# Kernel tuning notes

Hardware: AMD Instinct MI355X
Metric: run time of the kernel (lower is better)

The kernel has to match this reference:

```python
import jax, jax.numpy as jnp
import numpy as np

DIM = 512
HEADS = 8
DIM_HEAD = 64
INNER = HEADS * DIM_HEAD          # 512
CPB_DIM = DIM // 2                # 256 (ContinuousPositionBias hidden dim)
FF_INNER = int(DIM * 4 * 2 / 3)   # 1365 (GEGLU inner dim)
B, C, F, H, W = 2, 512, 8, 32, 32
SCALE = DIM_HEAD ** -0.5


def setup_inputs() -> dict:
    key = jax.random.key(0)
    ks = jax.random.split(key, 24)
    def rnd(k, shape, s=0.02):
        return jax.random.normal(k, shape, jnp.float32) * s
    return {
        "x": jax.random.normal(ks[0], (B, C, F, W, W), jnp.float32)[:, :, :, :H, :],
        # spatial attention
        "sa_gamma": jnp.ones((DIM,), jnp.float32),
        "sa_wq": rnd(ks[1], (DIM, INNER)),
        "sa_wkv": rnd(ks[2], (DIM, 2 * INNER)),
        "sa_wo": rnd(ks[3], (INNER, DIM)),
        # temporal attention
        "ta_gamma": jnp.ones((DIM,), jnp.float32),
        "ta_wq": rnd(ks[4], (DIM, INNER)),
        "ta_wkv": rnd(ks[5], (DIM, 2 * INNER)),
        "ta_wo": rnd(ks[6], (INNER, DIM)),
        # spatial ContinuousPositionBias MLP (num_dims=2, layers=2)
        "sp_w1": rnd(ks[7], (2, CPB_DIM), 0.1), "sp_b1": jnp.zeros((CPB_DIM,), jnp.float32),
        "sp_w2": rnd(ks[8], (CPB_DIM, CPB_DIM), 0.05), "sp_b2": jnp.zeros((CPB_DIM,), jnp.float32),
        "sp_w3": rnd(ks[9], (CPB_DIM, HEADS), 0.05), "sp_b3": jnp.zeros((HEADS,), jnp.float32),
        # temporal ContinuousPositionBias MLP (num_dims=1)
        "tp_w1": rnd(ks[10], (1, CPB_DIM), 0.1), "tp_b1": jnp.zeros((CPB_DIM,), jnp.float32),
        "tp_w2": rnd(ks[11], (CPB_DIM, CPB_DIM), 0.05), "tp_b2": jnp.zeros((CPB_DIM,), jnp.float32),
        "tp_w3": rnd(ks[12], (CPB_DIM, HEADS), 0.05), "tp_b3": jnp.zeros((HEADS,), jnp.float32),
        # FeedForward: Conv3d 1x1 (no bias) -> GEGLU -> RMSNorm -> Conv3d 1x1
        "ff_win": rnd(ks[13], (DIM, 2 * FF_INNER)),
        "ff_gamma": jnp.ones((FF_INNER,), jnp.float32),
        "ff_wout": rnd(ks[14], (FF_INNER, DIM)),
    }


def _rms_last(x, g):
    # torch: F.normalize(x, dim=-1) * sqrt(C) * gamma
    nrm = jnp.sqrt(jnp.sum(x * x, axis=-1, keepdims=True))
    return x / jnp.maximum(nrm, 1e-12) * jnp.sqrt(jnp.float32(x.shape[-1])) * g


def _mlp_bias(rel, w1, b1, w2, b2, w3, b3):
    h = jax.nn.silu(rel @ w1 + b1)
    h = jax.nn.silu(h @ w2 + b2)
    return h @ w3 + b3  # [R, heads]


def _cpb_2d(h, w, params):
    ry = jnp.arange(-(h - 1), h, dtype=jnp.float32)
    rx = jnp.arange(-(w - 1), w, dtype=jnp.float32)
    gy, gx = jnp.meshgrid(ry, rx, indexing='ij')
    rel = jnp.stack([gy, gx], -1).reshape(-1, 2)          # [(2h-1)(2w-1), 2]
    tab = _mlp_bias(rel, *params)                          # [R, heads]
    py, px = jnp.meshgrid(jnp.arange(h), jnp.arange(w), indexing='ij')
    pos = jnp.stack([py.reshape(-1), px.reshape(-1)], -1)  # [n, 2]
    d = pos[:, None, :] - pos[None, :, :]                  # [n, n, 2]
    idx = (d[..., 0] + h - 1) * (2 * w - 1) + (d[..., 1] + w - 1)
    return jnp.transpose(tab[idx], (2, 0, 1))              # [heads, n, n]


def _cpb_1d(f, params):
    rel = jnp.arange(-(f - 1), f, dtype=jnp.float32)[:, None]
    tab = _mlp_bias(rel, *params)                          # [2f-1, heads]
    p = jnp.arange(f)
    idx = p[:, None] - p[None, :] + f - 1
    return jnp.transpose(tab[idx], (2, 0, 1))              # [heads, f, f]


def _attn(x, gamma, wq, wkv, wo, bias):
    # x: [b, n, c]; manual softmax(QK^T*scale + bias)V (flash disabled by pos_bias)
    xn = _rms_last(x, gamma)
    q = xn @ wq
    k, v = jnp.split(xn @ wkv, 2, axis=-1)
    b, n, _ = q.shape
    rs = lambda t: t.reshape(b, n, HEADS, DIM_HEAD).transpose(0, 2, 1, 3)
    q, k, v = rs(q), rs(k), rs(v)
    s = jnp.einsum('bhid,bhjd->bhij', q, k) * SCALE + bias[None]
    a = jax.nn.softmax(s, axis=-1)
    o = jnp.einsum('bhij,bhjd->bhid', a, v)
    o = o.transpose(0, 2, 1, 3).reshape(b, n, INNER)
    return o @ wo


def _ff(x, win, gamma, wout):
    # x: [b, f, h, w, c] channel-last; Conv3d 1x1 == channel einsum
    hdn = jnp.einsum('bfhwc,co->bfhwo', x, win)
    a, gate = jnp.split(hdn, 2, axis=-1)
    y = a * jax.nn.gelu(gate, approximate=False)           # GEGLU (torch exact gelu)
    # shift_token: chunk channels, shift second half by +1 frame
    c1 = (FF_INNER + 1) // 2
    t1, t2 = y[..., :c1], y[..., c1:]
    t2 = jnp.pad(t2, ((0, 0), (1, 0), (0, 0), (0, 0), (0, 0)))[:, :-1]
    y = jnp.concatenate([t1, t2], axis=-1)
    yn = _rms_last(y, gamma)                               # RMSNorm over channels
    return jnp.einsum('bfhwi,ic->bfhwc', yn, wout)


def reference(x, sa_gamma, sa_wq, sa_wkv, sa_wo, ta_gamma, ta_wq, ta_wkv, ta_wo,
              sp_w1, sp_b1, sp_w2, sp_b2, sp_w3, sp_b3,
              tp_w1, tp_b1, tp_w2, tp_b2, tp_w3, tp_b3,
              ff_win, ff_gamma, ff_wout):
    b, c, f, h, w = x.shape
    xl = jnp.transpose(x, (0, 2, 3, 4, 1))                 # b f h w c
    # spatial attention over (h w) tokens, batched over (b f)
    xs = xl.reshape(b * f, h * w, c)
    sp_bias = _cpb_2d(h, w, (sp_w1, sp_b1, sp_w2, sp_b2, sp_w3, sp_b3))
    xs = _attn(xs, sa_gamma, sa_wq, sa_wkv, sa_wo, sp_bias) + xs
    xv = xs.reshape(b, f, h, w, c)
    # temporal attention over f tokens, batched over (b h w)
    xt = jnp.transpose(xv, (0, 2, 3, 1, 4)).reshape(b * h * w, f, c)
    tp_bias = _cpb_1d(f, (tp_w1, tp_b1, tp_w2, tp_b2, tp_w3, tp_b3))
    xt = _attn(xt, ta_gamma, ta_wq, ta_wkv, ta_wo, tp_bias) + xt
    xv = jnp.transpose(xt.reshape(b, h, w, f, c), (0, 3, 1, 2, 4))
    # GEGLU feedforward with token shift
    xv = _ff(xv, ff_win, ff_gamma, ff_wout) + xv
    return jnp.transpose(xv, (0, 4, 1, 2, 3))              # b c f h w
```

## Files before the change

kernel.cpp:

```cpp
#include <hip/hip_runtime.h>
#include <cstdint>
#include <cstddef>

typedef __bf16 bf16_t;
typedef __bf16 bf16x8 __attribute__((ext_vector_type(8)));
typedef __bf16 bf16x4 __attribute__((ext_vector_type(4)));
typedef float floatx4 __attribute__((ext_vector_type(4)));

__device__ __forceinline__ float wred_sum(float v) {
#pragma unroll
  for (int off = 32; off > 0; off >>= 1) v += __shfl_xor(v, off);
  return v;
}
__device__ __forceinline__ void async16(const void* g, void* l) {
  __builtin_amdgcn_global_load_lds((const __attribute__((address_space(1))) void*)g,
                                   (__attribute__((address_space(3))) void*)l, 16, 0, 0);
}

template <int MODE>
__global__ __launch_bounds__(256) void st_gemm(
    const bf16_t* __restrict__ A, const bf16_t* __restrict__ B, void* Cp, void* Cp2,
    const float* Res, int M, int N, int K, int lda, int ldb, int ldc) {
  __shared__ bf16_t sA[3][128 * 32];
  __shared__ bf16_t sB[3][128 * 32];
  const int tid = threadIdx.x;
  const int bm = blockIdx.x, bn = blockIdx.y;
  const int lane = tid & 63;
  const int wave = tid >> 6;
  const int wm = (wave >> 1) * 64, wn = (wave & 1) * 64;
  const int rowf = lane & 15, qc = lane >> 4;
  const int fco = (qc ^ ((rowf >> 1) & 3)) * 8;

  const bf16_t* aSrc[2];
  const bf16_t* bSrc[2];
  int sOff[2];
#pragma unroll
  for (int it = 0; it < 2; ++it) {
    int slot = it * 256 + tid;
    int mi = slot >> 2, kc = slot & 3;
    int cs = kc ^ ((mi >> 1) & 3);
    int ar = bm * 128 + mi; if (ar > M - 1) ar = M - 1;
    int br = bn * 128 + mi; if (br > N - 1) br = N - 1;
    aSrc[it] = A + (size_t)ar * lda + cs * 8;
    bSrc[it] = B + (size_t)br * ldb + cs * 8;
    sOff[it] = slot * 16;
  }

  floatx4 acc[4][4];
#pragma unroll
  for (int i = 0; i < 4; ++i)
#pragma unroll
    for (int j = 0; j < 4; ++j) acc[i][j] = floatx4{0.f, 0.f, 0.f, 0.f};

  const int NT = K >> 5;
#pragma unroll
  for (int it = 0; it < 2; ++it) {
    async16(aSrc[it], (char*)sA[0] + sOff[it]);
    async16(bSrc[it], (char*)sB[0] + sOff[it]);
  }
#pragma unroll
  for (int it = 0; it < 2; ++it) {
    async16(aSrc[it] + 32, (char*)sA[1] + sOff[it]);
    async16(bSrc[it] + 32, (char*)sB[1] + sOff[it]);
  }
  __builtin_amdgcn_sched_barrier(0);
  asm volatile("s_waitcnt vmcnt(4)" ::: "memory");
  __builtin_amdgcn_s_barrier();
  __builtin_amdgcn_sched_barrier(0);

  int bcur = 0, bnx = 2;
#pragma unroll 1
  for (int t = 0; t < NT; ++t) {
    const bf16_t* sAc = sA[bcur];
    const bf16_t* sBc = sB[bcur];
    bf16x8 af[4], bv[4];
#pragma unroll
    for (int i = 0; i < 4; ++i) {
      af[i] = *(const bf16x8*)(sAc + (wm + i * 16 + rowf) * 32 + fco);
      bv[i] = *(const bf16x8*)(sBc + (wn + i * 16 + rowf) * 32 + fco);
    }
    if (t + 2 < NT) {
      const int kt2 = (t + 2) * 32;
#pragma unroll
      for (int it = 0; it < 2; ++it) {
        async16(aSrc[it] + kt2, (char*)sA[bnx] + sOff[it]);
        async16(bSrc[it] + kt2, (char*)sB[bnx] + sOff[it]);
      }
    }
#pragma unroll
    for (int i = 0; i < 4; ++i)
#pragma unroll
      for (int j = 0; j < 4; ++j)
        acc[i][j] = __builtin_amdgcn_mfma_f32_16x16x32_bf16(af[i], bv[j], acc[i][j], 0, 0, 0);
    if (t + 1 < NT) {
      __builtin_amdgcn_sched_barrier(0);
      if (t + 2 < NT) asm volatile("s_waitcnt vmcnt(4)" ::: "memory");
      else            asm volatile("s_waitcnt vmcnt(0)" ::: "memory");
      __builtin_amdgcn_s_barrier();
      __builtin_amdgcn_sched_barrier(0);
    }
    bcur = (bcur == 2) ? 0 : bcur + 1;
    bnx = (bnx == 2) ? 0 : bnx + 1;
  }

  const int cl = lane & 15;
  const int rowBase = bm * 128 + wm + (lane >> 4) * 4;
  if (MODE == 5) {
    bf16_t* yb = (bf16_t*)Cp;
    const int cg0 = ((bn * 128 + wn) >> 5) * 16;
#pragma unroll
    for (int i = 0; i < 4; ++i) {
#pragma unroll
      for (int p = 0; p < 2; ++p) {
        int c = cg0 + p * 16 + cl;
        if (c >= 1365) continue;
#pragma unroll
        for (int r = 0; r < 4; ++r) {
          int row = rowBase + i * 16 + r;
          if (row >= M) continue;
          float a = acc[i][2 * p][r];
          float gt = acc[i][2 * p + 1][r];
          float zz = gt * (0.7978845608f + 0.03567740814f * gt * gt);
          float u = __builtin_exp2f(-2.8853900817779268f * zz);
          float y = a * gt / (1.f + u);
          yb[(size_t)row * ldc + c] = (bf16_t)y;
        }
      }
    }
    return;
  }
  const int colBase = bn * 128 + wn + cl;
#pragma unroll
  for (int i = 0; i < 4; ++i) {
#pragma unroll
    for (int j = 0; j < 4; ++j) {
      int col = colBase + j * 16;
      if (col >= N) continue;
#pragma unroll
      for (int r = 0; r < 4; ++r) {
        int row = rowBase + i * 16 + r;
        if (row >= M) continue;
        long long inidx = (long long)row * ldc + col;
        float v = acc[i][j][r];
        if (MODE >= 2) v += Res[inidx];
        if (MODE == 1) { ((bf16_t*)Cp)[inidx] = (bf16_t)v; }
        else if (MODE == 2) { ((float*)Cp)[inidx] = v; }
        else if (MODE == 3) {
          int orow = (row & ~8191) | ((row & 1023) << 3) | ((row >> 10) & 7);
          ((float*)Cp)[(long long)orow * ldc + col] = v;
        } else if (MODE == 4) {
          int orow = (row & ~8191) | ((row & 7) << 10) | ((row >> 3) & 1023);
          long long oidx = (long long)orow * ldc + col;
          ((float*)Cp)[oidx] = v;
          ((bf16_t*)Cp2)[oidx] = (bf16_t)v;
        }
      }
    }
  }
}

__global__ __launch_bounds__(256) void st_transpose2d(
    const float* __restrict__ in, float* __restrict__ out, int R, int Cc,
    long long inb, long long outb) {
  __shared__ float tile[32][33];
  const int ct = blockIdx.x, rt = blockIdx.y, b = blockIdx.z;
  in += (long long)b * inb;
  out += (long long)b * outb;
  const int tx = threadIdx.x & 31, ty = threadIdx.x >> 5;
#pragma unroll
  for (int k = 0; k < 4; ++k) {
    int r = rt * 32 + ty + k * 8;
    int c = ct * 32 + tx;
    tile[ty + k * 8][tx] = in[(size_t)r * Cc + c];
  }
  __syncthreads();
#pragma unroll
  for (int k = 0; k < 4; ++k) {
    int c = ct * 32 + ty + k * 8;
    int r = rt * 32 + tx;
    out[(size_t)c * R + r] = tile[tx][ty + k * 8];
  }
}

__global__ void st_wtrans(const float* __restrict__ src, bf16_t* __restrict__ dst,
                          int K, int Kpad, int N, int srcld, int coloff, long total) {
  long idx = (long)blockIdx.x * 256 + threadIdx.x;
  if (idx >= total) return;
  int kp = (int)(idx % Kpad);
  int n = (int)(idx / Kpad);
  float v = (kp < K) ? src[(size_t)kp * srcld + coloff + n] : 0.f;
  dst[idx] = (bf16_t)v;
}

__global__ void st_wtrans_geglu(const float* __restrict__ src, bf16_t* __restrict__ dst,
                                long total) {
  long idx = (long)blockIdx.x * 256 + threadIdx.x;
  if (idx >= total) return;
  int kp = (int)(idx & 511);
  int n = (int)(idx >> 9);
  int c = ((n >> 5) << 4) + (n & 15);
  float v = 0.f;
  if (c < 1365) {
    int srccol = c + (((n >> 4) & 1) ? 1365 : 0);
    v = src[(size_t)kp * 2730 + srccol];
  }
  dst[idx] = (bf16_t)v;
}

__global__ __launch_bounds__(256) void st_cpb(
    const float* __restrict__ w1, const float* __restrict__ b1,
    const float* __restrict__ w2, const float* __restrict__ b2,
    const float* __restrict__ w3, const float* __restrict__ b3,
    float* __restrict__ tab2d, float* __restrict__ tab1d, int two_d) {
  const int pos = blockIdx.x, t = threadIdx.x;
  float r0, r1 = 0.f;
  if (two_d) { r0 = (float)(pos / 63 - 31); r1 = (float)(pos % 63 - 31); }
  else { r0 = (float)(pos - 7); }
  __shared__ float sh[256];
  float h = r0 * w1[t] + (two_d ? r1 * w1[256 + t] : 0.f) + b1[t];
  h = h / (1.f + expf(-h));
  sh[t] = h;
  __syncthreads();
  float h2 = b2[t];
  for (int j = 0; j < 256; ++j) h2 += sh[j] * w2[j * 256 + t];
  h2 = h2 / (1.f + expf(-h2));
  __syncthreads();
  sh[t] = h2;
  __syncthreads();
  if (t < 8) {
    float o = b3[t];
    for (int j = 0; j < 256; ++j) o += sh[j] * w3[j * 8 + t];
    if (two_d) tab2d[t * 4000 + pos] = o * 8.0f;
    else tab1d[t * 15 + pos] = o;
  }
}

__global__ __launch_bounds__(256) void st_rmsnorm(const float* __restrict__ x,
                                                  const float* __restrict__ gamma,
                                                  bf16_t* __restrict__ y) {
  const int token = blockIdx.x * 4 + (threadIdx.x >> 6);
  const int lane = threadIdx.x & 63;
  const float* xr = x + (size_t)token * 512;
  float v[8];
  float ss = 0.f;
#pragma unroll
  for (int k = 0; k < 8; ++k) { v[k] = xr[k * 64 + lane]; ss += v[k] * v[k]; }
  ss = wred_sum(ss);
  const float r = 22.627416998f / fmaxf(sqrtf(ss), 1e-12f);
  bf16_t* yr = y + (size_t)token * 512;
#pragma unroll
  for (int k = 0; k < 8; ++k) yr[k * 64 + lane] = (bf16_t)(v[k] * r * gamma[k * 64 + lane]);
}

__global__ __launch_bounds__(256) void st_vtrans(const bf16_t* __restrict__ qkv,
                                                 bf16_t* __restrict__ vT) {
  __shared__ float tile[32][33];
  const int jt = blockIdx.x, dt = blockIdx.y, z = blockIdx.z;
  const int bf = z >> 3, h = z & 7;
  const int tx = threadIdx.x & 31, ty = threadIdx.x >> 5;
#pragma unroll
  for (int k = 0; k < 4; ++k) {
    int j = jt * 32 + ty + k * 8;
    int d = dt * 32 + tx;
    tile[ty + k * 8][tx] = (float)qkv[((size_t)(bf * 1024 + j)) * 1536 + 1024 + h * 64 + d];
  }
  __syncthreads();
#pragma unroll
  for (int k = 0; k < 4; ++k) {
    int d = dt * 32 + ty + k * 8;
    int j = jt * 32 + tx;
    vT[((size_t)z * 64 + d) * 1024 + j] = (bf16_t)tile[tx][ty + k * 8];
  }
}

__global__ __launch_bounds__(256, 4) void st_flash(
    const bf16_t* __restrict__ qkv, const bf16_t* __restrict__ vT,
    const float* __restrict__ tab2f, bf16_t* __restrict__ ob) {
  __shared__ __align__(16) bf16_t ldsK[3][32 * 64];
  __shared__ __align__(16) char ldsP[4 * 32 * 80];
  __shared__ __align__(16) float ldsT[2208];
  const int z = blockIdx.x;
  const int qtile = blockIdx.y;
  const int bf = z >> 3, h = z & 7;
  const int tid = threadIdx.x;
  const int lane = tid & 63, wave = tid >> 6;
  const int cl = lane & 15, g = lane >> 4;
  const size_t qkvBase = (size_t)bf * 1024 * 1536 + h * 64;
  const int eoff = (qtile * 252) & ~3;
  const bf16_t* Kp = qkv + qkvBase + 512;
  const bf16_t* Vp = vT + (size_t)z * 65536;

#pragma unroll
  for (int it = 0; it < 3; ++it) {
    int s = it * 256 + tid;
    if (s < 552) async16(tab2f + h * 4000 + eoff + s * 4, (char*)ldsT + s * 16);
  }
  const int krow = tid >> 3, kc = tid & 7;
  const bf16_t* kSrc = Kp + (size_t)krow * 1536 + (kc ^ (krow & 7)) * 8;
  async16(kSrc, (char*)ldsK[0] + tid * 16);
  async16(kSrc + (size_t)32 * 1536, (char*)ldsK[1] + tid * 16);
  bf16x8 aq[2][2];
#pragma unroll
  for (int it = 0; it < 2; ++it)
#pragma unroll
    for (int ks = 0; ks < 2; ++ks) {
      int row = qtile * 128 + wave * 32 + it * 16 + cl;
      aq[it][ks] = *(const bf16x8*)(qkv + qkvBase + (size_t)row * 1536 + (ks * 4 + g) * 8);
    }
  const bf16_t* vPtr[4];
#pragma unroll
  for (int dt = 0; dt < 4; ++dt) vPtr[dt] = Vp + (size_t)(dt * 16 + cl) * 1024 + g * 8;
  __syncthreads();

  int fiB[2];
#pragma unroll
  for (int it = 0; it < 2; ++it) {
    int i = qtile * 128 + wave * 32 + it * 16 + cl;
    fiB[it] = (i >> 5) * 63 + (i & 31) + 1984 - eoff;
  }
  float lsum[2] = {0.f, 0.f};
  floatx4 oacc[4][2];
#pragma unroll
  for (int dt = 0; dt < 4; ++dt)
#pragma unroll
    for (int it = 0; it < 2; ++it) oacc[dt][it] = floatx4{0.f, 0.f, 0.f, 0.f};

  char* ldsPw = ldsP + wave * 2560;
  const float SC = 0.18033688011112042f;

  int bcur = 0, bnx = 2;
#pragma unroll 1
  for (int t = 0; t < 32; ++t) {
    const bf16_t* Kc = ldsK[bcur];
    const int j0 = t * 32;
#pragma unroll
    for (int jt = 0; jt < 2; ++jt) {
      int jb = j0 + jt * 16 + g * 4;
      int fjb = (jb >> 5) * 63 + (jb & 31);
      floatx4 sj[2];
#pragma unroll
      for (int it = 0; it < 2; ++it) {
        int idx0 = fiB[it] - fjb;
        sj[it] = floatx4{ldsT[idx0], ldsT[idx0 - 1], ldsT[idx0 - 2], ldsT[idx0 - 3]};
      }
#pragma unroll
      for (int ks = 0; ks < 2; ++ks) {
        int row = jt * 16 + cl;
        bf16x8 kf = *(const bf16x8*)(Kc + row * 64 + (((ks * 4 + g) ^ (row & 7))) * 8);
#pragma unroll
        for (int it = 0; it < 2; ++it)
          sj[it] = __builtin_amdgcn_mfma_f32_16x16x32_bf16(kf, aq[it][ks], sj[it], 0, 0, 0);
      }
#pragma unroll
      for (int it = 0; it < 2; ++it) {
        float e0 = __builtin_exp2f(sj[it][0] * SC);
        float e1 = __builtin_exp2f(sj[it][1] * SC);
        float e2 = __builtin_exp2f(sj[it][2] * SC);
        float e3 = __builtin_exp2f(sj[it][3] * SC);
        lsum[it] += (e0 + e1) + (e2 + e3);
        bf16x4 pv = {(bf16_t)e0, (bf16_t)e1, (bf16_t)e2, (bf16_t)e3};
        *(bf16x4*)(ldsPw + (it * 16 + cl) * 80 + (jt * 4 + g) * 8) = pv;
      }
    }
    {
      bf16x8 pB[2];
#pragma unroll
      for (int it = 0; it < 2; ++it)
        pB[it] = *(const bf16x8*)(ldsPw + (it * 16 + cl) * 80 + g * 16);
#pragma unroll
      for (int dt = 0; dt < 4; ++dt) {
        bf16x8 vf = *(const bf16x8*)(vPtr[dt] + j0);
#pragma unroll
        for (int it = 0; it < 2; ++it)
          oacc[dt][it] = __builtin_amdgcn_mfma_f32_16x16x32_bf16(vf, pB[it], oacc[dt][it], 0, 0, 0);
      }
    }
    if (t + 2 < 32) async16(kSrc + (size_t)(t + 2) * 32 * 1536, (char*)ldsK[bnx] + tid * 16);
    if (t + 1 < 32) {
      __builtin_amdgcn_sched_barrier(0);
      if (t + 2 < 32) asm volatile("s_waitcnt vmcnt(1)" ::: "memory");
      else            asm volatile("s_waitcnt vmcnt(0)" ::: "memory");
      __builtin_amdgcn_s_barrier();
      __builtin_amdgcn_sched_barrier(0);
    }
    bcur = (bcur == 2) ? 0 : bcur + 1;
    bnx = (bnx == 2) ? 0 : bnx + 1;
  }
  float inv[2];
#pragma unroll
  for (int it = 0; it < 2; ++it) {
    float s = lsum[it];
    s += __shfl_xor(s, 16);
    s += __shfl_xor(s, 32);
    inv[it] = 1.f / s;
  }
#pragma unroll
  for (int it = 0; it < 2; ++it) {
    int i = qtile * 128 + wave * 32 + it * 16 + cl;
    size_t base = ((size_t)bf * 1024 + i) * 512 + h * 64 + g * 4;
#pragma unroll
    for (int dt = 0; dt < 4; ++dt) {
      bf16x4 ov = {(bf16_t)(oacc[dt][it][0] * inv[it]), (bf16_t)(oacc[dt][it][1] * inv[it]),
                   (bf16_t)(oacc[dt][it][2] * inv[it]), (bf16_t)(oacc[dt][it][3] * inv[it])};
      *(bf16x4*)(ob + base + dt * 16) = ov;
    }
  }
}

__global__ __launch_bounds__(256) void st_tattn2(const bf16_t* __restrict__ qkv,
                                                 const float* __restrict__ tabf,
                                                 bf16_t* __restrict__ o) {
  const int wg = blockIdx.x * 4 + (threadIdx.x >> 6);
  const int bhw = wg >> 3, head = wg & 7;
  const int lane = threadIdx.x & 63;
  const size_t base = (size_t)bhw * 8 * 1536 + head * 64 + lane;
  float q[8], k[8], v[8];
#pragma unroll
  for (int f = 0; f < 8; ++f) {
    q[f] = (float)qkv[base + (size_t)f * 1536];
    k[f] = (float)qkv[base + (size_t)f * 1536 + 512];
    v[f] = (float)qkv[base + (size_t)f * 1536 + 1024];
  }
  float p[64];
#pragma unroll
  for (int i = 0; i < 8; ++i)
#pragma unroll
    for (int j = 0; j < 8; ++j) p[i * 8 + j] = q[i] * k[j];
#pragma unroll
  for (int st = 32; st >= 1; st >>= 1) {
    const bool hi = (lane & st) != 0;
#pragma unroll
    for (int m = 0; m < st; ++m) {
      float give = hi ? p[m] : p[m + st];
      float keep = hi ? p[m + st] : p[m];
      p[m] = keep + __shfl_xor(give, st);
    }
  }
  const int i = lane >> 3, j = lane & 7;
  float e = __expf(p[0] * 0.125f + tabf[head * 15 + i - j + 7]);
  float sm = e;
  sm += __shfl_xor(sm, 1);
  sm += __shfl_xor(sm, 2);
  sm += __shfl_xor(sm, 4);
  const float prob = e / sm;
  float acc[8];
#pragma unroll
  for (int ii = 0; ii < 8; ++ii) acc[ii] = 0.f;
#pragma unroll
  for (int ii = 0; ii < 8; ++ii)
#pragma unroll
    for (int jj = 0; jj < 8; ++jj)
      acc[ii] += __shfl(prob, ii * 8 + jj) * v[jj];
#pragma unroll
  for (int ii = 0; ii < 8; ++ii)
    o[(size_t)(bhw * 8 + ii) * 512 + head * 64 + lane] = (bf16_t)acc[ii];
}

__global__ __launch_bounds__(256) void st_glu(const bf16_t* __restrict__ y,
                                              const float* __restrict__ gamma,
                                              bf16_t* __restrict__ yn) {
  const int t = blockIdx.x;
  const int tid = threadIdx.x;
  const int f = (t >> 10) & 7;
  float yv[6];
  float ss = 0.f;
#pragma unroll
  for (int kk = 0; kk < 6; ++kk) {
    int c = kk * 256 + tid;
    float v = 0.f;
    if (c < 1365) {
      long src = t;
      bool valid = true;
      if (c >= 683) { if (f == 0) valid = false; else src = t - 1024; }
      if (valid) v = (float)y[src * 1365 + c];
    }
    yv[kk] = v;
    ss += v * v;
  }
  __shared__ float red[4];
  ss = wred_sum(ss);
  if ((tid & 63) == 0) red[tid >> 6] = ss;
  __syncthreads();
  ss = red[0] + red[1] + red[2] + red[3];
  const float r = sqrtf(1365.f) / fmaxf(sqrtf(ss), 1e-12f);
#pragma unroll
  for (int kk = 0; kk < 6; ++kk) {
    int c = kk * 256 + tid;
    if (c < 1365) yn[(size_t)t * 1376 + c] = (bf16_t)(yv[kk] * r * gamma[c]);
  }
  if (tid < 11) yn[(size_t)t * 1376 + 1365 + tid] = (bf16_t)0.f;
}

extern "C" void kernel_launch(void* const* d_in, const int* in_sizes, int n_in,
                              void* d_out, int out_size, void* d_ws, size_t ws_size,
                              hipStream_t stream) {
  const float* x        = (const float*)d_in[0];
  const float* sa_gamma = (const float*)d_in[1];
  const float* sa_wq    = (const float*)d_in[2];
  const float* sa_wkv   = (const float*)d_in[3];
  const float* sa_wo    = (const float*)d_in[4];
  const float* ta_gamma = (const float*)d_in[5];
  const float* ta_wq    = (const float*)d_in[6];
  const float* ta_wkv   = (const float*)d_in[7];
  const float* ta_wo    = (const float*)d_in[8];
  const float* sp_w1 = (const float*)d_in[9];
  const float* sp_b1 = (const float*)d_in[10];
  const float* sp_w2 = (const float*)d_in[11];
  const float* sp_b2 = (const float*)d_in[12];
  const float* sp_w3 = (const float*)d_in[13];
  const float* sp_b3 = (const float*)d_in[14];
  const float* tp_w1 = (const float*)d_in[15];
  const float* tp_b1 = (const float*)d_in[16];
  const float* tp_w2 = (const float*)d_in[17];
  const float* tp_b2 = (const float*)d_in[18];
  const float* tp_w3 = (const float*)d_in[19];
  const float* tp_b3 = (const float*)d_in[20];
  const float* ff_win   = (const float*)d_in[21];
  const float* ff_gamma = (const float*)d_in[22];
  const float* ff_wout  = (const float*)d_in[23];
  float* outp = (float*)d_out;

  char* ws = (char*)d_ws;
  size_t off = 0;
  auto alloc = [&](size_t bytes) -> char* {
    char* p = ws + off;
    off += (bytes + 255) & ~(size_t)255;
    return p;
  };
  const long T = 16384;
  float*  xs  = (float*)alloc((size_t)T * 512 * 4);
  bf16_t* xn  = (bf16_t*)alloc((size_t)T * 512 * 2);
  char*   R2  = alloc((size_t)T * 1536 * 2);
  char*   R3  = alloc((size_t)T * 1536 * 2);
  char*   R4  = alloc((size_t)T * 1376 * 2);
  bf16_t* wqkvT_sa = (bf16_t*)alloc(1536ULL * 512 * 2);
  bf16_t* woT_sa   = (bf16_t*)alloc(512ULL * 512 * 2);
  bf16_t* wqkvT_ta = (bf16_t*)alloc(1536ULL * 512 * 2);
  bf16_t* woT_ta   = (bf16_t*)alloc(512ULL * 512 * 2);
  bf16_t* winT  = (bf16_t*)alloc(2752ULL * 512 * 2);
  bf16_t* woutT = (bf16_t*)alloc(512ULL * 1376 * 2);
  float*  tab2f = (float*)alloc(8 * 4000 * 4);
  float*  tabf  = (float*)alloc(8 * 15 * 4);

  bf16_t* qkv  = (bf16_t*)R2;
  bf16_t* ybuf = (bf16_t*)R2;
  bf16_t* vT   = (bf16_t*)R3;
  float*  xt   = (float*)R3;
  bf16_t* ob_s = xn;
  bf16_t* ob_t = (bf16_t*)R4;
  bf16_t* ynb  = (bf16_t*)R4;

  st_transpose2d<<<dim3(256, 16, 2), 256, 0, stream>>>(x, xs, 512, 8192,
                                                       (long long)512 * 8192, (long long)512 * 8192);
  auto wt = [&](const float* src, bf16_t* dst, int K, int Kpad, int N, int srcld, int coloff) {
    long tot = (long)N * Kpad;
    st_wtrans<<<dim3((tot + 255) / 256), 256, 0, stream>>>(src, dst, K, Kpad, N, srcld, coloff, tot);
  };
  wt(sa_wq, wqkvT_sa, 512, 512, 512, 512, 0);
  wt(sa_wkv, wqkvT_sa + 512 * 512, 512, 512, 1024, 1024, 0);
  wt(sa_wo, woT_sa, 512, 512, 512, 512, 0);
  wt(ta_wq, wqkvT_ta, 512, 512, 512, 512, 0);
  wt(ta_wkv, wqkvT_ta + 512 * 512, 512, 512, 1024, 1024, 0);
  wt(ta_wo, woT_ta, 512, 512, 512, 512, 0);
  st_wtrans_geglu<<<dim3((2752 * 512) / 256), 256, 0, stream>>>(ff_win, winT, 2752L * 512);
  wt(ff_wout, woutT, 1365, 1376, 512, 512, 0);
  st_cpb<<<dim3(3969), 256, 0, stream>>>(sp_w1, sp_b1, sp_w2, sp_b2, sp_w3, sp_b3, tab2f, tabf, 1);
  st_cpb<<<dim3(15), 256, 0, stream>>>(tp_w1, tp_b1, tp_w2, tp_b2, tp_w3, tp_b3, tab2f, tabf, 0);

  st_rmsnorm<<<dim3(4096), 256, 0, stream>>>(xs, sa_gamma, xn);
  st_gemm<1><<<dim3(128, 12), 256, 0, stream>>>(
      xn, wqkvT_sa, (void*)qkv, nullptr, nullptr, 16384, 1536, 512, 512, 512, 1536);
  st_vtrans<<<dim3(32, 2, 128), 256, 0, stream>>>(qkv, vT);
  st_flash<<<dim3(128, 8), 256, 0, stream>>>(qkv, vT, tab2f, ob_s);
  st_gemm<3><<<dim3(128, 4), 256, 0, stream>>>(
      ob_s, woT_sa, (void*)xt, nullptr, xs, 16384, 512, 512, 512, 512, 512);

  st_rmsnorm<<<dim3(4096), 256, 0, stream>>>(xt, ta_gamma, xn);
  st_gemm<1><<<dim3(128, 12), 256, 0, stream>>>(
      xn, wqkvT_ta, (void*)qkv, nullptr, nullptr, 16384, 1536, 512, 512, 512, 1536);
  st_tattn2<<<dim3(4096), 256, 0, stream>>>(qkv, tabf, ob_t);
  st_gemm<4><<<dim3(128, 4), 256, 0, stream>>>(
      ob_t, woT_ta, (void*)xs, (void*)xn, xt, 16384, 512, 512, 512, 512, 512);

  st_gemm<5><<<dim3(128, 22), 256, 0, stream>>>(
      xn, winT, (void*)ybuf, nullptr, nullptr, 16384, 2752, 512, 512, 512, 1365);
  st_glu<<<dim3(16384), 256, 0, stream>>>(ybuf, ff_gamma, ynb);
  st_gemm<2><<<dim3(128, 4), 256, 0, stream>>>(
      ynb, woutT, (void*)xs, nullptr, xs, 16384, 512, 1376, 1376, 1376, 512);

  st_transpose2d<<<dim3(16, 256, 2), 256, 0, stream>>>(xs, outp, 8192, 512,
                                                       (long long)8192 * 512, (long long)8192 * 512);
}
```

Baseline: 658.0 us.

## Use wider 128x256 GEMM tile for GEGLU projection and fold softmax scale into Q

Adds a dedicated GEGLU input-projection GEMM with a 128x256 output tile (4x8 MFMA accumulators per wave, launch bounds of 2 blocks per CU). It takes over from the 128x128 MODE 5 path, with the weight padding enlarged to 2816 rows. This aims to improve operand reuse per LDS load and cut the block count. Separately, the attention scale times log2(e) is now applied to Q in the QKV GEMM epilogue, and the position-bias tables are pre-multiplied by log2(e), which removes per-score multiplies in both attention kernels. The wider tile raises register pressure and can limit occupancy, and scaling Q before the bf16 rounding slightly changes numerics.

```diff
diff --git a/kernel.cpp b/kernel.cpp
--- a/kernel.cpp
+++ b/kernel.cpp
@@ -16,6 +16,8 @@
   __builtin_amdgcn_global_load_lds((const __attribute__((address_space(1))) void*)g,
                                    (__attribute__((address_space(3))) void*)l, 16, 0, 0);
 }
+
+#define QSCALE 0.18033688011112042f
 
 template <int MODE>
 __global__ __launch_bounds__(256) void st_gemm(
@@ -105,30 +107,6 @@
 
   const int cl = lane & 15;
   const int rowBase = bm * 128 + wm + (lane >> 4) * 4;
-  if (MODE == 5) {
-    bf16_t* yb = (bf16_t*)Cp;
-    const int cg0 = ((bn * 128 + wn) >> 5) * 16;
-#pragma unroll
-    for (int i = 0; i < 4; ++i) {
-#pragma unroll
-      for (int p = 0; p < 2; ++p) {
-        int c = cg0 + p * 16 + cl;
-        if (c >= 1365) continue;
-#pragma unroll
-        for (int r = 0; r < 4; ++r) {
-          int row = rowBase + i * 16 + r;
-          if (row >= M) continue;
-          float a = acc[i][2 * p][r];
-          float gt = acc[i][2 * p + 1][r];
-          float zz = gt * (0.7978845608f + 0.03567740814f * gt * gt);
-          float u = __builtin_exp2f(-2.8853900817779268f * zz);
-          float y = a * gt / (1.f + u);
-          yb[(size_t)row * ldc + c] = (bf16_t)y;
-        }
-      }
-    }
-    return;
-  }
   const int colBase = bn * 128 + wn + cl;
 #pragma unroll
   for (int i = 0; i < 4; ++i) {
@@ -142,8 +120,9 @@
         if (row >= M) continue;
         long long inidx = (long long)row * ldc + col;
         float v = acc[i][j][r];
-        if (MODE >= 2) v += Res[inidx];
+        if (MODE >= 2 && MODE <= 4) v += Res[inidx];
         if (MODE == 1) { ((bf16_t*)Cp)[inidx] = (bf16_t)v; }
+        else if (MODE == 6) { ((bf16_t*)Cp)[inidx] = (bf16_t)(col < 512 ? v * QSCALE : v); }
         else if (MODE == 2) { ((float*)Cp)[inidx] = v; }
         else if (MODE == 3) {
           int orow = (row & ~8191) | ((row & 1023) << 3) | ((row >> 10) & 7);
@@ -154,6 +133,119 @@
           ((float*)Cp)[oidx] = v;
           ((bf16_t*)Cp2)[oidx] = (bf16_t)v;
         }
+      }
+    }
+  }
+}
+
+__global__ __launch_bounds__(256, 2) void st_gemmW(
+    const bf16_t* __restrict__ A, const bf16_t* __restrict__ B, bf16_t* __restrict__ yb,
+    int M, int N, int K, int lda, int ldb, int ldc) {
+  __shared__ bf16_t sA[3][128 * 32];
+  __shared__ bf16_t sB[3][256 * 32];
+  const int tid = threadIdx.x;
+  const int bm = blockIdx.x, bn = blockIdx.y;
+  const int lane = tid & 63;
+  const int wave = tid >> 6;
+  const int wr = wave >> 1, wc = wave & 1;
+  const int rowf = lane & 15, qc = lane >> 4;
+  const int fco = (qc ^ ((rowf >> 1) & 3)) * 8;
+
+  const bf16_t* aSrc[2];
+  const bf16_t* bSrc[4];
+  int aOff[2], bOff[4];
+#pragma unroll
+  for (int it = 0; it < 2; ++it) {
+    int slot = it * 256 + tid;
+    int mi = slot >> 2, kc = slot & 3;
+    int cs = kc ^ ((mi >> 1) & 3);
+    aSrc[it] = A + (size_t)(bm * 128 + mi) * lda + cs * 8;
+    aOff[it] = slot * 16;
+  }
+#pragma unroll
+  for (int it = 0; it < 4; ++it) {
+    int slot = it * 256 + tid;
+    int mi = slot >> 2, kc = slot & 3;
+    int cs = kc ^ ((mi >> 1) & 3);
+    int br = bn * 256 + mi; if (br > N - 1) br = N - 1;
+    bSrc[it] = B + (size_t)br * ldb + cs * 8;
+    bOff[it] = slot * 16;
+  }
+
+  floatx4 acc[4][8];
+#pragma unroll
+  for (int i = 0; i < 4; ++i)
+#pragma unroll
+    for (int j = 0; j < 8; ++j) acc[i][j] = floatx4{0.f, 0.f, 0.f, 0.f};
+
+  const int NT = K >> 5;
+#pragma unroll
+  for (int tt = 0; tt < 2; ++tt) {
+#pragma unroll
+    for (int it = 0; it < 2; ++it) async16(aSrc[it] + tt * 32, (char*)sA[tt] + aOff[it]);
+#pragma unroll
+    for (int it = 0; it < 4; ++it) async16(bSrc[it] + tt * 32, (char*)sB[tt] + bOff[it]);
+  }
+  __builtin_amdgcn_sched_barrier(0);
+  asm volatile("s_waitcnt vmcnt(6)" ::: "memory");
+  __builtin_amdgcn_s_barrier();
+  __builtin_amdgcn_sched_barrier(0);
+
+  int bcur = 0, bnx = 2;
+#pragma unroll 1
+  for (int t = 0; t < NT; ++t) {
+    const bf16_t* sAc = sA[bcur];
+    const bf16_t* sBc = sB[bcur];
+    bf16x8 af[4], bv[8];
+#pragma unroll
+    for (int i = 0; i < 4; ++i)
+      af[i] = *(const bf16x8*)(sAc + (wr * 64 + i * 16 + rowf) * 32 + fco);
+#pragma unroll
+    for (int j = 0; j < 8; ++j)
+      bv[j] = *(const bf16x8*)(sBc + (wc * 128 + j * 16 + rowf) * 32 + fco);
+    if (t + 2 < NT) {
+      const int kt2 = (t + 2) * 32;
+#pragma unroll
+      for (int it = 0; it < 2; ++it) async16(aSrc[it] + kt2, (char*)sA[bnx] + aOff[it]);
+#pragma unroll
+      for (int it = 0; it < 4; ++it) async16(bSrc[it] + kt2, (char*)sB[bnx] + bOff[it]);
+    }
+    __builtin_amdgcn_s_setprio(1);
+#pragma unroll
+    for (int i = 0; i < 4; ++i)
+#pragma unroll
+      for (int j = 0; j < 8; ++j)
+        acc[i][j] = __builtin_amdgcn_mfma_f32_16x16x32_bf16(af[i], bv[j], acc[i][j], 0, 0, 0);
+    __builtin_amdgcn_s_setprio(0);
+    if (t + 1 < NT) {
+      __builtin_amdgcn_sched_barrier(0);
+      if (t + 2 < NT) asm volatile("s_waitcnt vmcnt(6)" ::: "memory");
+      else            asm volatile("s_waitcnt vmcnt(0)" ::: "memory");
+      __builtin_amdgcn_s_barrier();
+      __builtin_amdgcn_sched_barrier(0);
+    }
+    bcur = (bcur == 2) ? 0 : bcur + 1;
+    bnx = (bnx == 2) ? 0 : bnx + 1;
+  }
+
+  const int cl = lane & 15, g = lane >> 4;
+  const int rowBase = bm * 128 + wr * 64 + g * 4;
+  const int cg0 = (bn * 8 + wc * 4) * 16;
+#pragma unroll
+  for (int i = 0; i < 4; ++i) {
+#pragma unroll
+    for (int p = 0; p < 4; ++p) {
+      int c = cg0 + p * 16 + cl;
+      if (c >= 1365) continue;
+#pragma unroll
+      for (int r = 0; r < 4; ++r) {
+        int row = rowBase + i * 16 + r;
+        float a = acc[i][2 * p][r];
+        float gt = acc[i][2 * p + 1][r];
+        float zz = gt * (0.7978845608f + 0.03567740814f * gt * gt);
+        float u = __builtin_exp2f(-2.8853900817779268f * zz);
+        float y = a * gt / (1.f + u);
+        yb[(size_t)row * ldc + c] = (bf16_t)y;
       }
     }
   }
@@ -230,8 +322,8 @@
   if (t < 8) {
     float o = b3[t];
     for (int j = 0; j < 256; ++j) o += sh[j] * w3[j * 8 + t];
-    if (two_d) tab2d[t * 4000 + pos] = o * 8.0f;
-    else tab1d[t * 15 + pos] = o;
+    if (two_d) tab2d[t * 4000 + pos] = o * 1.4426950408889634f;
+    else tab1d[t * 15 + pos] = o * 1.4426950408889634f;
   }
 }
 
@@ -326,7 +418,6 @@
     for (int it = 0; it < 2; ++it) oacc[dt][it] = floatx4{0.f, 0.f, 0.f, 0.f};
 
   char* ldsPw = ldsP + wave * 2560;
-  const float SC = 0.18033688011112042f;
 
   int bcur = 0, bnx = 2;
 #pragma unroll 1
@@ -353,10 +444,10 @@
       }
 #pragma unroll
       for (int it = 0; it < 2; ++it) {
-        float e0 = __builtin_exp2f(sj[it][0] * SC);
-        float e1 = __builtin_exp2f(sj[it][1] * SC);
-        float e2 = __builtin_exp2f(sj[it][2] * SC);
-        float e3 = __builtin_exp2f(sj[it][3] * SC);
+        float e0 = __builtin_exp2f(sj[it][0]);
+        float e1 = __builtin_exp2f(sj[it][1]);
+        float e2 = __builtin_exp2f(sj[it][2]);
+        float e3 = __builtin_exp2f(sj[it][3]);
         lsum[it] += (e0 + e1) + (e2 + e3);
         bf16x4 pv = {(bf16_t)e0, (bf16_t)e1, (bf16_t)e2, (bf16_t)e3};
         *(bf16x4*)(ldsPw + (it * 16 + cl) * 80 + (jt * 4 + g) * 8) = pv;
@@ -437,7 +528,7 @@
     }
   }
   const int i = lane >> 3, j = lane & 7;
-  float e = __expf(p[0] * 0.125f + tabf[head * 15 + i - j + 7]);
+  float e = __builtin_exp2f(p[0] + tabf[head * 15 + i - j + 7]);
   float sm = e;
   sm += __shfl_xor(sm, 1);
   sm += __shfl_xor(sm, 2);
@@ -537,7 +628,7 @@
   bf16_t* woT_sa   = (bf16_t*)alloc(512ULL * 512 * 2);
   bf16_t* wqkvT_ta = (bf16_t*)alloc(1536ULL * 512 * 2);
   bf16_t* woT_ta   = (bf16_t*)alloc(512ULL * 512 * 2);
-  bf16_t* winT  = (bf16_t*)alloc(2752ULL * 512 * 2);
+  bf16_t* winT  = (bf16_t*)alloc(2816ULL * 512 * 2);
   bf16_t* woutT = (bf16_t*)alloc(512ULL * 1376 * 2);
   float*  tab2f = (float*)alloc(8 * 4000 * 4);
   float*  tabf  = (float*)alloc(8 * 15 * 4);
@@ -562,13 +653,13 @@
   wt(ta_wq, wqkvT_ta, 512, 512, 512, 512, 0);
   wt(ta_wkv, wqkvT_ta + 512 * 512, 512, 512, 1024, 1024, 0);
   wt(ta_wo, woT_ta, 512, 512, 512, 512, 0);
-  st_wtrans_geglu<<<dim3((2752 * 512) / 256), 256, 0, stream>>>(ff_win, winT, 2752L * 512);
+  st_wtrans_geglu<<<dim3((2816 * 512) / 256), 256, 0, stream>>>(ff_win, winT, 2816L * 512);
   wt(ff_wout, woutT, 1365, 1376, 512, 512, 0);
   st_cpb<<<dim3(3969), 256, 0, stream>>>(sp_w1, sp_b1, sp_w2, sp_b2, sp_w3, sp_b3, tab2f, tabf, 1);
   st_cpb<<<dim3(15), 256, 0, stream>>>(tp_w1, tp_b1, tp_w2, tp_b2, tp_w3, tp_b3, tab2f, tabf, 0);
 
   st_rmsnorm<<<dim3(4096), 256, 0, stream>>>(xs, sa_gamma, xn);
-  st_gemm<1><<<dim3(128, 12), 256, 0, stream>>>(
+  st_gemm<6><<<dim3(128, 12), 256, 0, stream>>>(
       xn, wqkvT_sa, (void*)qkv, nullptr, nullptr, 16384, 1536, 512, 512, 512, 1536);
   st_vtrans<<<dim3(32, 2, 128), 256, 0, stream>>>(qkv, vT);
   st_flash<<<dim3(128, 8), 256, 0, stream>>>(qkv, vT, tab2f, ob_s);
@@ -576,14 +667,14 @@
       ob_s, woT_sa, (void*)xt, nullptr, xs, 16384, 512, 512, 512, 512, 512);
 
   st_rmsnorm<<<dim3(4096), 256, 0, stream>>>(xt, ta_gamma, xn);
-  st_gemm<1><<<dim3(128, 12), 256, 0, stream>>>(
+  st_gemm<6><<<dim3(128, 12), 256, 0, stream>>>(
       xn, wqkvT_ta, (void*)qkv, nullptr, nullptr, 16384, 1536, 512, 512, 512, 1536);
   st_tattn2<<<dim3(4096), 256, 0, stream>>>(qkv, tabf, ob_t);
   st_gemm<4><<<dim3(128, 4), 256, 0, stream>>>(
       ob_t, woT_ta, (void*)xs, (void*)xn, xt, 16384, 512, 512, 512, 512, 512);
 
-  st_gemm<5><<<dim3(128, 22), 256, 0, stream>>>(
-      xn, winT, (void*)ybuf, nullptr, nullptr, 16384, 2752, 512, 512, 512, 1365);
+  st_gemmW<<<dim3(128, 11), 256, 0, stream>>>(
+      xn, winT, ybuf, 16384, 2816, 512, 512, 512, 1365);
   st_glu<<<dim3(16384), 256, 0, stream>>>(ybuf, ff_gamma, ynb);
   st_gemm<2><<<dim3(128, 4), 256, 0, stream>>>(
       ynb, woutT, (void*)xs, nullptr, xs, 16384, 512, 1376, 1376, 1376, 512);
```

After: 662.7 us. No clear change (+0.7%).

## Prepack GEMM weights in MFMA fragment order and fold softmax scale into Q

Applied to the files above, without the earlier changes.

Weight transpose kernels now write B in a pre-swizzled layout grouped by 16-column fragment and K-tile, so each lane of the GEMM loads its MFMA B operand straight from global memory with one 16-byte load. The B LDS buffers and their async copies are dropped, which halves LDS traffic and staging per K-step. The attention scale and log2(e) are folded into Q in a new QKV-GEMM epilogue and into the bias tables, removing per-element multiplies from the flash and temporal softmax. The cost is that B loads are no longer shared through LDS: each wave fetches its fragments from global memory or cache, and their latency is not covered by the async prefetch pipeline.

```diff
diff --git a/kernel.cpp b/kernel.cpp
--- a/kernel.cpp
+++ b/kernel.cpp
@@ -17,12 +17,13 @@
                                    (__attribute__((address_space(3))) void*)l, 16, 0, 0);
 }
 
+#define QSCALE 0.18033688011112042f
+
 template <int MODE>
 __global__ __launch_bounds__(256) void st_gemm(
-    const bf16_t* __restrict__ A, const bf16_t* __restrict__ B, void* Cp, void* Cp2,
-    const float* Res, int M, int N, int K, int lda, int ldb, int ldc) {
+    const bf16_t* __restrict__ A, const bf16_t* __restrict__ Bf, void* Cp, void* Cp2,
+    const float* Res, int M, int N, int K, int lda, int nt, int ldc) {
   __shared__ bf16_t sA[3][128 * 32];
-  __shared__ bf16_t sB[3][128 * 32];
   const int tid = threadIdx.x;
   const int bm = blockIdx.x, bn = blockIdx.y;
   const int lane = tid & 63;
@@ -32,7 +33,6 @@
   const int fco = (qc ^ ((rowf >> 1) & 3)) * 8;
 
   const bf16_t* aSrc[2];
-  const bf16_t* bSrc[2];
   int sOff[2];
 #pragma unroll
   for (int it = 0; it < 2; ++it) {
@@ -40,11 +40,15 @@
     int mi = slot >> 2, kc = slot & 3;
     int cs = kc ^ ((mi >> 1) & 3);
     int ar = bm * 128 + mi; if (ar > M - 1) ar = M - 1;
-    int br = bn * 128 + mi; if (br > N - 1) br = N - 1;
     aSrc[it] = A + (size_t)ar * lda + cs * 8;
-    bSrc[it] = B + (size_t)br * ldb + cs * 8;
     sOff[it] = slot * 16;
   }
+  const bf16_t* bPtr[4];
+#pragma unroll
+  for (int j = 0; j < 4; ++j) {
+    int ngrp = bn * 8 + (wn >> 4) + j;
+    bPtr[j] = Bf + (size_t)ngrp * nt * 512 + lane * 8;
+  }
 
   floatx4 acc[4][4];
 #pragma unroll
@@ -53,18 +57,12 @@
     for (int j = 0; j < 4; ++j) acc[i][j] = floatx4{0.f, 0.f, 0.f, 0.f};
 
   const int NT = K >> 5;
-#pragma unroll
-  for (int it = 0; it < 2; ++it) {
-    async16(aSrc[it], (char*)sA[0] + sOff[it]);
-    async16(bSrc[it], (char*)sB[0] + sOff[it]);
-  }
-#pragma unroll
-  for (int it = 0; it < 2; ++it) {
-    async16(aSrc[it] + 32, (char*)sA[1] + sOff[it]);
-    async16(bSrc[it] + 32, (char*)sB[1] + sOff[it]);
-  }
+  async16(aSrc[0], (char*)sA[0] + sOff[0]);
+  async16(aSrc[1], (char*)sA[0] + sOff[1]);
+  async16(aSrc[0] + 32, (char*)sA[1] + sOff[0]);
+  async16(aSrc[1] + 32, (char*)sA[1] + sOff[1]);
   __builtin_amdgcn_sched_barrier(0);
-  asm volatile("s_waitcnt vmcnt(4)" ::: "memory");
+  asm volatile("s_waitcnt vmcnt(2)" ::: "memory");
   __builtin_amdgcn_s_barrier();
   __builtin_amdgcn_sched_barrier(0);
 
@@ -72,20 +70,16 @@
 #pragma unroll 1
   for (int t = 0; t < NT; ++t) {
     const bf16_t* sAc = sA[bcur];
-    const bf16_t* sBc = sB[bcur];
     bf16x8 af[4], bv[4];
 #pragma unroll
-    for (int i = 0; i < 4; ++i) {
+    for (int j = 0; j < 4; ++j) bv[j] = *(const bf16x8*)(bPtr[j] + (size_t)t * 512);
+#pragma unroll
+    for (int i = 0; i < 4; ++i)
       af[i] = *(const bf16x8*)(sAc + (wm + i * 16 + rowf) * 32 + fco);
-      bv[i] = *(const bf16x8*)(sBc + (wn + i * 16 + rowf) * 32 + fco);
-    }
     if (t + 2 < NT) {
       const int kt2 = (t + 2) * 32;
 #pragma unroll
-      for (int it = 0; it < 2; ++it) {
-        async16(aSrc[it] + kt2, (char*)sA[bnx] + sOff[it]);
-        async16(bSrc[it] + kt2, (char*)sB[bnx] + sOff[it]);
-      }
+      for (int it = 0; it < 2; ++it) async16(aSrc[it] + kt2, (char*)sA[bnx] + sOff[it]);
     }
 #pragma unroll
     for (int i = 0; i < 4; ++i)
@@ -94,7 +88,7 @@
         acc[i][j] = __builtin_amdgcn_mfma_f32_16x16x32_bf16(af[i], bv[j], acc[i][j], 0, 0, 0);
     if (t + 1 < NT) {
       __builtin_amdgcn_sched_barrier(0);
-      if (t + 2 < NT) asm volatile("s_waitcnt vmcnt(4)" ::: "memory");
+      if (t + 2 < NT) asm volatile("s_waitcnt vmcnt(2)" ::: "memory");
       else            asm volatile("s_waitcnt vmcnt(0)" ::: "memory");
       __builtin_amdgcn_s_barrier();
       __builtin_amdgcn_sched_barrier(0);
@@ -117,7 +111,6 @@
 #pragma unroll
         for (int r = 0; r < 4; ++r) {
           int row = rowBase + i * 16 + r;
-          if (row >= M) continue;
           float a = acc[i][2 * p][r];
           float gt = acc[i][2 * p + 1][r];
           float zz = gt * (0.7978845608f + 0.03567740814f * gt * gt);
@@ -142,8 +135,9 @@
         if (row >= M) continue;
         long long inidx = (long long)row * ldc + col;
         float v = acc[i][j][r];
-        if (MODE >= 2) v += Res[inidx];
+        if (MODE >= 2 && MODE <= 4) v += Res[inidx];
         if (MODE == 1) { ((bf16_t*)Cp)[inidx] = (bf16_t)v; }
+        else if (MODE == 6) { ((bf16_t*)Cp)[inidx] = (bf16_t)(col < 512 ? v * QSCALE : v); }
         else if (MODE == 2) { ((float*)Cp)[inidx] = v; }
         else if (MODE == 3) {
           int orow = (row & ~8191) | ((row & 1023) << 3) | ((row >> 10) & 7);
@@ -189,7 +183,9 @@
   int kp = (int)(idx % Kpad);
   int n = (int)(idx / Kpad);
   float v = (kp < K) ? src[(size_t)kp * srcld + coloff + n] : 0.f;
-  dst[idx] = (bf16_t)v;
+  int t = kp >> 5, kc = (kp >> 3) & 3, e = kp & 7;
+  long daddr = ((long)(n >> 4) * (Kpad >> 5) + t) * 512 + ((kc << 4) + (n & 15)) * 8 + e;
+  dst[daddr] = (bf16_t)v;
 }
 
 __global__ void st_wtrans_geglu(const float* __restrict__ src, bf16_t* __restrict__ dst,
@@ -204,7 +200,9 @@
     int srccol = c + (((n >> 4) & 1) ? 1365 : 0);
     v = src[(size_t)kp * 2730 + srccol];
   }
-  dst[idx] = (bf16_t)v;
+  int t = kp >> 5, kc = (kp >> 3) & 3, e = kp & 7;
+  long daddr = ((long)(n >> 4) * 16 + t) * 512 + ((kc << 4) + (n & 15)) * 8 + e;
+  dst[daddr] = (bf16_t)v;
 }
 
 __global__ __launch_bounds__(256) void st_cpb(
@@ -230,8 +228,8 @@
   if (t < 8) {
     float o = b3[t];
     for (int j = 0; j < 256; ++j) o += sh[j] * w3[j * 8 + t];
-    if (two_d) tab2d[t * 4000 + pos] = o * 8.0f;
-    else tab1d[t * 15 + pos] = o;
+    if (two_d) tab2d[t * 4000 + pos] = o * 1.4426950408889634f;
+    else tab1d[t * 15 + pos] = o * 1.4426950408889634f;
   }
 }
 
@@ -326,7 +324,6 @@
     for (int it = 0; it < 2; ++it) oacc[dt][it] = floatx4{0.f, 0.f, 0.f, 0.f};
 
   char* ldsPw = ldsP + wave * 2560;
-  const float SC = 0.18033688011112042f;
 
   int bcur = 0, bnx = 2;
 #pragma unroll 1
@@ -353,10 +350,10 @@
       }
 #pragma unroll
       for (int it = 0; it < 2; ++it) {
-        float e0 = __builtin_exp2f(sj[it][0] * SC);
-        float e1 = __builtin_exp2f(sj[it][1] * SC);
-        float e2 = __builtin_exp2f(sj[it][2] * SC);
-        float e3 = __builtin_exp2f(sj[it][3] * SC);
+        float e0 = __builtin_exp2f(sj[it][0]);
+        float e1 = __builtin_exp2f(sj[it][1]);
+        float e2 = __builtin_exp2f(sj[it][2]);
+        float e3 = __builtin_exp2f(sj[it][3]);
         lsum[it] += (e0 + e1) + (e2 + e3);
         bf16x4 pv = {(bf16_t)e0, (bf16_t)e1, (bf16_t)e2, (bf16_t)e3};
         *(bf16x4*)(ldsPw + (it * 16 + cl) * 80 + (jt * 4 + g) * 8) = pv;
@@ -437,7 +434,7 @@
     }
   }
   const int i = lane >> 3, j = lane & 7;
-  float e = __expf(p[0] * 0.125f + tabf[head * 15 + i - j + 7]);
+  float e = __builtin_exp2f(p[0] + tabf[head * 15 + i - j + 7]);
   float sm = e;
   sm += __shfl_xor(sm, 1);
   sm += __shfl_xor(sm, 2);
@@ -537,7 +534,7 @@
   bf16_t* woT_sa   = (bf16_t*)alloc(512ULL * 512 * 2);
   bf16_t* wqkvT_ta = (bf16_t*)alloc(1536ULL * 512 * 2);
   bf16_t* woT_ta   = (bf16_t*)alloc(512ULL * 512 * 2);
-  bf16_t* winT  = (bf16_t*)alloc(2752ULL * 512 * 2);
+  bf16_t* winT  = (bf16_t*)alloc(2816ULL * 512 * 2);
   bf16_t* woutT = (bf16_t*)alloc(512ULL * 1376 * 2);
   float*  tab2f = (float*)alloc(8 * 4000 * 4);
   float*  tabf  = (float*)alloc(8 * 15 * 4);
@@ -562,31 +559,31 @@
   wt(ta_wq, wqkvT_ta, 512, 512, 512, 512, 0);
   wt(ta_wkv, wqkvT_ta + 512 * 512, 512, 512, 1024, 1024, 0);
   wt(ta_wo, woT_ta, 512, 512, 512, 512, 0);
-  st_wtrans_geglu<<<dim3((2752 * 512) / 256), 256, 0, stream>>>(ff_win, winT, 2752L * 512);
+  st_wtrans_geglu<<<dim3((2816 * 512) / 256), 256, 0, stream>>>(ff_win, winT, 2816L * 512);
   wt(ff_wout, woutT, 1365, 1376, 512, 512, 0);
   st_cpb<<<dim3(3969), 256, 0, stream>>>(sp_w1, sp_b1, sp_w2, sp_b2, sp_w3, sp_b3, tab2f, tabf, 1);
   st_cpb<<<dim3(15), 256, 0, stream>>>(tp_w1, tp_b1, tp_w2, tp_b2, tp_w3, tp_b3, tab2f, tabf, 0);
 
   st_rmsnorm<<<dim3(4096), 256, 0, stream>>>(xs, sa_gamma, xn);
-  st_gemm<1><<<dim3(128, 12), 256, 0, stream>>>(
-      xn, wqkvT_sa, (void*)qkv, nullptr, nullptr, 16384, 1536, 512, 512, 512, 1536);
+  st_gemm<6><<<dim3(128, 12), 256, 0, stream>>>(
+      xn, wqkvT_sa, (void*)qkv, nullptr, nullptr, 16384, 1536, 512, 512, 16, 1536);
   st_vtrans<<<dim3(32, 2, 128), 256, 0, stream>>>(qkv, vT);
   st_flash<<<dim3(128, 8), 256, 0, stream>>>(qkv, vT, tab2f, ob_s);
   st_gemm<3><<<dim3(128, 4), 256, 0, stream>>>(
-      ob_s, woT_sa, (void*)xt, nullptr, xs, 16384, 512, 512, 512, 512, 512);
+      ob_s, woT_sa, (void*)xt, nullptr, xs, 16384, 512, 512, 512, 16, 512);
 
   st_rmsnorm<<<dim3(4096), 256, 0, stream>>>(xt, ta_gamma, xn);
-  st_gemm<1><<<dim3(128, 12), 256, 0, stream>>>(
-      xn, wqkvT_ta, (void*)qkv, nullptr, nullptr, 16384, 1536, 512, 512, 512, 1536);
+  st_gemm<6><<<dim3(128, 12), 256, 0, stream>>>(
+      xn, wqkvT_ta, (void*)qkv, nullptr, nullptr, 16384, 1536, 512, 512, 16, 1536);
   st_tattn2<<<dim3(4096), 256, 0, stream>>>(qkv, tabf, ob_t);
   st_gemm<4><<<dim3(128, 4), 256, 0, stream>>>(
-      ob_t, woT_ta, (void*)xs, (void*)xn, xt, 16384, 512, 512, 512, 512, 512);
+      ob_t, woT_ta, (void*)xs, (void*)xn, xt, 16384, 512, 512, 512, 16, 512);
 
   st_gemm<5><<<dim3(128, 22), 256, 0, stream>>>(
-      xn, winT, (void*)ybuf, nullptr, nullptr, 16384, 2752, 512, 512, 512, 1365);
+      xn, winT, (void*)ybuf, nullptr, nullptr, 16384, 2816, 512, 512, 16, 1365);
   st_glu<<<dim3(16384), 256, 0, stream>>>(ybuf, ff_gamma, ynb);
   st_gemm<2><<<dim3(128, 4), 256, 0, stream>>>(
-      ynb, woutT, (void*)xs, nullptr, xs, 16384, 512, 1376, 1376, 1376, 512);
+      ynb, woutT, (void*)xs, nullptr, xs, 16384, 512, 1376, 1376, 43, 512);
 
   st_transpose2d<<<dim3(16, 256, 2), 256, 0, stream>>>(xs, outp, 8192, 512,
                                                        (long long)8192 * 512, (long long)8192 * 512);
```

After: 667.7 us. About the same (+1.5%).
